# Kernel optimization log

Measured on AMD Instinct MI355X. Metric: run time of the kernel, lower is better.

The kernel has to match this reference:

```python
import jax, jax.numpy as jnp
import numpy as np

BATCH_SIZE = 4096
TEMPERATURE = 0.5
DIAG_NEG = -50000.0
EPS = 1e-8  # torch CosineSimilarity eps


def setup_inputs() -> dict:
    key = jax.random.key(0)
    k1, k2 = jax.random.split(key)
    z_i = jax.random.normal(k1, (BATCH_SIZE, 128), dtype=jnp.float32)
    z_j = jax.random.normal(k2, (BATCH_SIZE, 128), dtype=jnp.float32)
    return {"z_i": z_i, "z_j": z_j}


def reference(z_i, z_j):
    n = z_i.shape[0]
    z = jnp.concatenate([z_i, z_j], axis=0)  # [2N, D]
    # cosine similarity: normalize once, then one GEMM (same math as
    # CosineSimilarity(dim=2) on the broadcasted pair, with eps clamp on norms)
    norms = jnp.maximum(jnp.linalg.norm(z, axis=-1, keepdims=True), EPS)
    zn = z / norms
    sim = (zn @ zn.T) / TEMPERATURE  # [2N, 2N]
    # mask self-similarity on the diagonal
    idx = jnp.arange(2 * n)
    sim = sim.at[idx, idx].set(DIAG_NEG)
    # labels: positive pair is the other view
    labels = jnp.concatenate([idx[n:], idx[:n]])  # [2N]
    # mean softmax cross-entropy
    logp = jax.nn.log_softmax(sim, axis=-1)
    loss = -jnp.mean(logp[idx, labels])
    return loss
```

## Files before the change

kernel.cpp:

```cpp
#include <hip/hip_runtime.h>

#define N2 8192
#define NHALF 4096
#define DDIM 128
#define NCHUNK 16
#define CPC 512
#define NT 8
#define LN2F 0.69314718055994530942f
#define SCALEF 1.6986436f

typedef __attribute__((ext_vector_type(8))) short bf8_t;
typedef __attribute__((ext_vector_type(4))) float f4_t;

__device__ __forceinline__ float fexp2(float x) { return __builtin_amdgcn_exp2f(x); }
__device__ __forceinline__ float flog2(float x) { return __builtin_amdgcn_logf(x); }

__device__ __forceinline__ unsigned short f2bf(float f) {
  unsigned int x = __float_as_uint(f);
  x += 0x7fffu + ((x >> 16) & 1u);
  return (unsigned short)(x >> 16);
}
__device__ __forceinline__ float bf2f(unsigned short h) {
  return __uint_as_float(((unsigned int)h) << 16);
}

__global__ __launch_bounds__(256) void knorm(const float* __restrict__ zi,
                                             const float* __restrict__ zj,
                                             unsigned short* __restrict__ u,
                                             float* __restrict__ dhat) {
  const int lane = threadIdx.x & 63;
  const int row = blockIdx.x * 4 + (threadIdx.x >> 6);
  const float* src = (row < NHALF) ? (zi + (size_t)row * DDIM)
                                   : (zj + (size_t)(row - NHALF) * DDIM);
  float2 x = *(const float2*)(src + lane * 2);
  float ss = x.x * x.x + x.y * x.y;
#pragma unroll
  for (int m = 32; m; m >>= 1) ss += __shfl_xor(ss, m);
  float scale = SCALEF / fmaxf(sqrtf(ss), 1e-8f);
  unsigned short b0 = f2bf(x.x * scale);
  unsigned short b1 = f2bf(x.y * scale);
  *(unsigned int*)(u + (size_t)row * DDIM + lane * 2) =
      (unsigned int)b0 | ((unsigned int)b1 << 16);
  float f0 = bf2f(b0), f1 = bf2f(b1);
  float dd = f0 * f0 + f1 * f1;
#pragma unroll
  for (int m = 32; m; m >>= 1) dd += __shfl_xor(dd, m);
  if (lane == 0) dhat[row] = dd;
}

__global__ __launch_bounds__(256) void ksim(const unsigned short* __restrict__ u,
                                            float* __restrict__ Lp) {
  __shared__ short Bls[24576];
  const int tid = threadIdx.x;
  const int lane = tid & 63;
  const int w = tid >> 6;
  const int rb = blockIdx.x >> 4;
  const int chunk = blockIdx.x & 15;
  const int lr = lane & 15, lq = lane >> 4;
  const int rowbase = rb * 256 + w * 64;
  const int colbase = chunk * CPC;

  bf8_t a[4][4];
#pragma unroll
  for (int s = 0; s < 4; s++)
#pragma unroll
    for (int kc = 0; kc < 4; kc++)
      a[s][kc] = *(const bf8_t*)(u + (size_t)(rowbase + s * 16 + lr) * DDIM +
                                 kc * 32 + lq * 8);
#pragma unroll
  for (int s = 0; s < 4; s++)
#pragma unroll
    for (int kc = 0; kc < 4; kc++)
      asm volatile("" : "+v"(a[s][kc]));

  f4_t L[4];
#pragma unroll
  for (int s = 0; s < 4; s++) L[s] = (f4_t){0.f, 0.f, 0.f, 0.f};

  auto STAGE = [&](int t) {
    const int bufo = (t % 3) * 8192;
#pragma unroll
    for (int i = 0; i < 4; i++) {
      const int j = w * 4 + i;
      const int col_local = j * 4 + lq;
      const int sdu = lr ^ (4 * (i & 1) + lq);
      const unsigned short* src =
          u + (size_t)(colbase + t * 64 + col_local) * DDIM + sdu * 8;
      short* dst = &Bls[bufo + j * 512];
      __builtin_amdgcn_global_load_lds(
          (const __attribute__((address_space(1))) unsigned int*)src,
          (__attribute__((address_space(3))) unsigned int*)dst, 16, 0, 0);
    }
  };

  auto COMP = [&](int t) {
    const short* P = &Bls[(t % 3) * 8192];
#pragma unroll
    for (int g = 0; g < 4; g++) {
      bf8_t bv[4];
#pragma unroll
      for (int kc = 0; kc < 4; kc++)
        bv[kc] = *(const bf8_t*)&P[((g * 16 + lr) * 16 +
                                    ((kc * 4 + lq) ^ (lr & 7))) * 8];
      f4_t acc[4];
#pragma unroll
      for (int s = 0; s < 4; s++) acc[s] = (f4_t){0.f, 0.f, 0.f, 0.f};
#pragma unroll
      for (int kc = 0; kc < 4; kc++)
#pragma unroll
        for (int s = 0; s < 4; s++)
          acc[s] = __builtin_amdgcn_mfma_f32_16x16x32_bf16(a[s][kc], bv[kc], acc[s], 0, 0, 0);
#pragma unroll
      for (int s = 0; s < 4; s++)
#pragma unroll
        for (int r = 0; r < 4; r++) L[s][r] += fexp2(acc[s][r]);
    }
  };

  STAGE(0);
  STAGE(1);
#pragma unroll 1
  for (int t = 0; t < NT; ++t) {
    if (t < NT - 1) {
      asm volatile("s_waitcnt vmcnt(4)" ::: "memory");
    } else {
      asm volatile("s_waitcnt vmcnt(0)" ::: "memory");
    }
    __builtin_amdgcn_sched_barrier(0);
    __builtin_amdgcn_s_barrier();
    __builtin_amdgcn_sched_barrier(0);
    COMP(t);
    if (t + 2 < NT) STAGE(t + 2);
  }

#pragma unroll
  for (int s = 0; s < 4; s++)
#pragma unroll
    for (int r = 0; r < 4; r++) {
      float v = L[s][r];
      v += __shfl_xor(v, 1); v += __shfl_xor(v, 2);
      v += __shfl_xor(v, 4); v += __shfl_xor(v, 8);
      if (lr == 0)
        Lp[(size_t)chunk * N2 + rowbase + s * 16 + lq * 4 + r] = v;
    }
}

__global__ __launch_bounds__(256) void krow(const unsigned short* __restrict__ u,
                                            const float* __restrict__ dhat,
                                            const float* __restrict__ Lp,
                                            float* __restrict__ bsum) {
  const int i = blockIdx.x * 256 + threadIdx.x;
  float L = 0.f;
#pragma unroll
  for (int c = 0; c < NCHUNK; c++) L += Lp[(size_t)c * N2 + i];
  L -= fexp2(dhat[i]);

  const int j = (i + NHALF) & (N2 - 1);
  const unsigned int* ui = (const unsigned int*)(u + (size_t)i * DDIM);
  const unsigned int* uj = (const unsigned int*)(u + (size_t)j * DDIM);
  float dot = 0.f;
#pragma unroll
  for (int k = 0; k < DDIM / 2; k++) {
    unsigned int av = ui[k], bv = uj[k];
    dot += __uint_as_float(av << 16) * __uint_as_float(bv << 16) +
           __uint_as_float(av & 0xffff0000u) * __uint_as_float(bv & 0xffff0000u);
  }
  float loss = LN2F * (flog2(L) - dot);

#pragma unroll
  for (int m = 32; m; m >>= 1) loss += __shfl_xor(loss, m);
  __shared__ float sred[4];
  if ((threadIdx.x & 63) == 0) sred[threadIdx.x >> 6] = loss;
  __syncthreads();
  if (threadIdx.x == 0) bsum[blockIdx.x] = sred[0] + sred[1] + sred[2] + sred[3];
}

__global__ void kfinal(const float* __restrict__ bsum, float* __restrict__ out) {
  float v = (threadIdx.x < N2 / 256) ? bsum[threadIdx.x] : 0.f;
#pragma unroll
  for (int m = 32; m; m >>= 1) v += __shfl_xor(v, m);
  if (threadIdx.x == 0) out[0] = v * (1.0f / N2);
}

extern "C" void kernel_launch(void* const* d_in, const int* in_sizes, int n_in,
                              void* d_out, int out_size, void* d_ws, size_t ws_size,
                              hipStream_t stream) {
  const float* zi = (const float*)d_in[0];
  const float* zj = (const float*)d_in[1];
  char* ws = (char*)d_ws;
  unsigned short* u = (unsigned short*)ws;
  float* dhat = (float*)(ws + (size_t)N2 * DDIM * 2);
  float* Lp = (float*)(ws + (size_t)N2 * DDIM * 2 + (size_t)N2 * 4);
  float* bsum = (float*)(ws + (size_t)N2 * DDIM * 2 + (size_t)N2 * 4 +
                         (size_t)NCHUNK * N2 * 4);
  float* out = (float*)d_out;

  hipLaunchKernelGGL(knorm, dim3(N2 / 4), dim3(256), 0, stream, zi, zj, u, dhat);
  hipLaunchKernelGGL(ksim, dim3((N2 / 256) * NCHUNK), dim3(256), 0, stream, u, Lp);
  hipLaunchKernelGGL(krow, dim3(N2 / 256), dim3(256), 0, stream, u, dhat, Lp, bsum);
  hipLaunchKernelGGL(kfinal, dim3(1), dim3(64), 0, stream, bsum, out);
}
```

Measured before the change: 40.57 us.

## Split ksim row tile across eight waves instead of four

The similarity kernel now launches 512 threads per block, with each wave owning 32 rows (two 16-row MFMA strips) instead of 64. The staging work for the shared B tile is split across eight waves, so each wave issues two async loads per stage, and the vmcnt wait is adjusted to match. This lowers per-wave register pressure and adds waves to hide exp and MFMA latency. In exchange each B fragment read from LDS is reused across fewer MFMAs, so LDS read traffic per FLOP doubles.

```diff
diff --git a/kernel.cpp b/kernel.cpp
--- a/kernel.cpp
+++ b/kernel.cpp
@@ -48,7 +48,7 @@
   if (lane == 0) dhat[row] = dd;
 }
 
-__global__ __launch_bounds__(256) void ksim(const unsigned short* __restrict__ u,
+__global__ __launch_bounds__(512) void ksim(const unsigned short* __restrict__ u,
                                             float* __restrict__ Lp) {
   __shared__ short Bls[24576];
   const int tid = threadIdx.x;
@@ -57,36 +57,33 @@
   const int rb = blockIdx.x >> 4;
   const int chunk = blockIdx.x & 15;
   const int lr = lane & 15, lq = lane >> 4;
-  const int rowbase = rb * 256 + w * 64;
+  const int rowbase = rb * 256 + w * 32;
   const int colbase = chunk * CPC;
 
-  bf8_t a[4][4];
-#pragma unroll
-  for (int s = 0; s < 4; s++)
+  bf8_t a[2][4];
+#pragma unroll
+  for (int s = 0; s < 2; s++)
 #pragma unroll
     for (int kc = 0; kc < 4; kc++)
       a[s][kc] = *(const bf8_t*)(u + (size_t)(rowbase + s * 16 + lr) * DDIM +
                                  kc * 32 + lq * 8);
 #pragma unroll
-  for (int s = 0; s < 4; s++)
+  for (int s = 0; s < 2; s++)
 #pragma unroll
     for (int kc = 0; kc < 4; kc++)
       asm volatile("" : "+v"(a[s][kc]));
 
-  f4_t L[4];
-#pragma unroll
-  for (int s = 0; s < 4; s++) L[s] = (f4_t){0.f, 0.f, 0.f, 0.f};
+  f4_t L0 = {0.f, 0.f, 0.f, 0.f}, L1 = {0.f, 0.f, 0.f, 0.f};
 
   auto STAGE = [&](int t) {
-    const int bufo = (t % 3) * 8192;
-#pragma unroll
-    for (int i = 0; i < 4; i++) {
-      const int j = w * 4 + i;
+#pragma unroll
+    for (int i = 0; i < 2; i++) {
+      const int j = w * 2 + i;
       const int col_local = j * 4 + lq;
-      const int sdu = lr ^ (4 * (i & 1) + lq);
+      const int sdu = lr ^ (4 * (j & 1) + lq);
       const unsigned short* src =
           u + (size_t)(colbase + t * 64 + col_local) * DDIM + sdu * 8;
-      short* dst = &Bls[bufo + j * 512];
+      short* dst = &Bls[(t % 3) * 8192 + j * 512];
       __builtin_amdgcn_global_load_lds(
           (const __attribute__((address_space(1))) unsigned int*)src,
           (__attribute__((address_space(3))) unsigned int*)dst, 16, 0, 0);
@@ -102,18 +99,17 @@
       for (int kc = 0; kc < 4; kc++)
         bv[kc] = *(const bf8_t*)&P[((g * 16 + lr) * 16 +
                                     ((kc * 4 + lq) ^ (lr & 7))) * 8];
-      f4_t acc[4];
-#pragma unroll
-      for (int s = 0; s < 4; s++) acc[s] = (f4_t){0.f, 0.f, 0.f, 0.f};
-#pragma unroll
-      for (int kc = 0; kc < 4; kc++)
-#pragma unroll
-        for (int s = 0; s < 4; s++)
-          acc[s] = __builtin_amdgcn_mfma_f32_16x16x32_bf16(a[s][kc], bv[kc], acc[s], 0, 0, 0);
-#pragma unroll
-      for (int s = 0; s < 4; s++)
-#pragma unroll
-        for (int r = 0; r < 4; r++) L[s][r] += fexp2(acc[s][r]);
+      f4_t acc0 = {0.f, 0.f, 0.f, 0.f}, acc1 = {0.f, 0.f, 0.f, 0.f};
+#pragma unroll
+      for (int kc = 0; kc < 4; kc++) {
+        acc0 = __builtin_amdgcn_mfma_f32_16x16x32_bf16(a[0][kc], bv[kc], acc0, 0, 0, 0);
+        acc1 = __builtin_amdgcn_mfma_f32_16x16x32_bf16(a[1][kc], bv[kc], acc1, 0, 0, 0);
+      }
+#pragma unroll
+      for (int r = 0; r < 4; r++) {
+        L0[r] += fexp2(acc0[r]);
+        L1[r] += fexp2(acc1[r]);
+      }
     }
   };
 
@@ -122,7 +118,7 @@
 #pragma unroll 1
   for (int t = 0; t < NT; ++t) {
     if (t < NT - 1) {
-      asm volatile("s_waitcnt vmcnt(4)" ::: "memory");
+      asm volatile("s_waitcnt vmcnt(2)" ::: "memory");
     } else {
       asm volatile("s_waitcnt vmcnt(0)" ::: "memory");
     }
@@ -134,15 +130,18 @@
   }
 
 #pragma unroll
-  for (int s = 0; s < 4; s++)
-#pragma unroll
-    for (int r = 0; r < 4; r++) {
-      float v = L[s][r];
-      v += __shfl_xor(v, 1); v += __shfl_xor(v, 2);
-      v += __shfl_xor(v, 4); v += __shfl_xor(v, 8);
-      if (lr == 0)
-        Lp[(size_t)chunk * N2 + rowbase + s * 16 + lq * 4 + r] = v;
-    }
+  for (int r = 0; r < 4; r++) {
+    float v0 = L0[r], v1 = L1[r];
+    v0 += __shfl_xor(v0, 1); v0 += __shfl_xor(v0, 2);
+    v0 += __shfl_xor(v0, 4); v0 += __shfl_xor(v0, 8);
+    v1 += __shfl_xor(v1, 1); v1 += __shfl_xor(v1, 2);
+    v1 += __shfl_xor(v1, 4); v1 += __shfl_xor(v1, 8);
+    if (lr == 0) {
+      const int rrow = rowbase + lq * 4 + r;
+      Lp[(size_t)chunk * N2 + rrow] = v0;
+      Lp[(size_t)chunk * N2 + rrow + 16] = v1;
+    }
+  }
 }
 
 __global__ __launch_bounds__(256) void krow(const unsigned short* __restrict__ u,
@@ -196,7 +195,7 @@
   float* out = (float*)d_out;
 
   hipLaunchKernelGGL(knorm, dim3(N2 / 4), dim3(256), 0, stream, zi, zj, u, dhat);
-  hipLaunchKernelGGL(ksim, dim3((N2 / 256) * NCHUNK), dim3(256), 0, stream, u, Lp);
+  hipLaunchKernelGGL(ksim, dim3((N2 / 256) * NCHUNK), dim3(512), 0, stream, u, Lp);
   hipLaunchKernelGGL(krow, dim3(N2 / 256), dim3(256), 0, stream, u, dhat, Lp, bsum);
   hipLaunchKernelGGL(kfinal, dim3(1), dim3(64), 0, stream, bsum, out);
 }
```

Result: faster. 37.54 us (-7.5%).
